# Kernel tuning notes

Measured on AMD Instinct MI355X. Metric: run time of the kernel, lower is better.

## Reference

```python
import jax, jax.numpy as jnp
import numpy as np

N_CLASSES = 18

def setup_inputs() -> dict:
    key = jax.random.key(0)
    k1, k2 = jax.random.split(key)
    B = 2_000_000
    output = jax.random.normal(k1, (B, N_CLASSES), dtype=jnp.float32)
    labels_soft = jax.random.uniform(k2, (B, N_CLASSES), dtype=jnp.float32)
    return {"output": output, "labels_soft": labels_soft}

def reference(output, labels_soft):
    # Original: sum over classes of mean_b( CE(output, cls) * labels_soft[:, cls] )
    # = mean over batch of sum_c( -log_softmax(output)[b, c] * labels_soft[b, c] )
    logp = jax.nn.log_softmax(output, axis=-1)          # [B, C]
    per_row = -jnp.sum(logp * labels_soft, axis=-1)     # [B]
    return jnp.mean(per_row)
```

## Files before the change

kernel.cpp:

```cpp
#include <hip/hip_runtime.h>

#define NCLS 18
#define RPC 128
#define CHF (RPC * NCLS)
#define CHF4 (CHF / 4)
#define WPB 4
#define GRID_A 1024

__global__ __launch_bounds__(256) void ce_soft_kernel(
    const float4* __restrict__ X4,
    const float4* __restrict__ L4,
    float* __restrict__ partials,
    int B)
{
    __shared__ float s[WPB][CHF];

    const int t    = threadIdx.x;
    const int lane = t & 63;
    const int wid  = t >> 6;
    const int gw   = blockIdx.x * WPB + wid;
    const int nw   = gridDim.x * WPB;
    const int nChunks = B / RPC;

    float acc = 0.0f;

    for (int ch = gw; ch < nChunks; ch += nw) {
        const size_t g4 = (size_t)ch * CHF4;
        float4 v[9];

        #pragma unroll
        for (int j = 0; j < 9; ++j) v[j] = X4[g4 + (size_t)(j * 64 + lane)];
        #pragma unroll
        for (int j = 0; j < 9; ++j) *(float4*)&s[wid][(j * 64 + lane) * 4] = v[j];
        __builtin_amdgcn_wave_barrier();

        float x0[NCLS], x1[NCLS];
        {
            const float2* r0 = (const float2*)&s[wid][(2 * lane)     * NCLS];
            const float2* r1 = (const float2*)&s[wid][(2 * lane + 1) * NCLS];
            #pragma unroll
            for (int j = 0; j < 9; ++j) {
                float2 a = r0[j]; x0[2*j] = a.x; x0[2*j+1] = a.y;
                float2 b = r1[j]; x1[2*j] = b.x; x1[2*j+1] = b.y;
            }
        }
        __builtin_amdgcn_wave_barrier();

        #pragma unroll
        for (int j = 0; j < 9; ++j) v[j] = L4[g4 + (size_t)(j * 64 + lane)];
        #pragma unroll
        for (int j = 0; j < 9; ++j) *(float4*)&s[wid][(j * 64 + lane) * 4] = v[j];

        float se0 = 0.0f, se1 = 0.0f;
        #pragma unroll
        for (int c = 0; c < NCLS; ++c) { se0 += __expf(x0[c]); se1 += __expf(x1[c]); }

        __builtin_amdgcn_wave_barrier();

        float dot0 = 0.0f, sl0 = 0.0f, dot1 = 0.0f, sl1 = 0.0f;
        {
            const float2* r0 = (const float2*)&s[wid][(2 * lane)     * NCLS];
            const float2* r1 = (const float2*)&s[wid][(2 * lane + 1) * NCLS];
            #pragma unroll
            for (int j = 0; j < 9; ++j) {
                float2 a = r0[j];
                dot0 = fmaf(a.x, x0[2*j], dot0); dot0 = fmaf(a.y, x0[2*j+1], dot0);
                sl0 += a.x + a.y;
                float2 b = r1[j];
                dot1 = fmaf(b.x, x1[2*j], dot1); dot1 = fmaf(b.y, x1[2*j+1], dot1);
                sl1 += b.x + b.y;
            }
        }
        acc += fmaf(sl0, __logf(se0), -dot0) + fmaf(sl1, __logf(se1), -dot1);
        __builtin_amdgcn_wave_barrier();
    }

    const float2* X2 = (const float2*)X4;
    const float2* L2 = (const float2*)L4;
    for (int row = nChunks * RPC + gw * 64 + lane; row < B; row += nw * 64) {
        float x[NCLS], l[NCLS];
        #pragma unroll
        for (int j = 0; j < 9; ++j) { float2 a = X2[(size_t)row * 9 + j]; x[2*j] = a.x; x[2*j+1] = a.y; }
        #pragma unroll
        for (int j = 0; j < 9; ++j) { float2 b = L2[(size_t)row * 9 + j]; l[2*j] = b.x; l[2*j+1] = b.y; }
        float se = 0.0f, dot = 0.0f, sl = 0.0f;
        #pragma unroll
        for (int c = 0; c < NCLS; ++c) { se += __expf(x[c]); dot = fmaf(l[c], x[c], dot); sl += l[c]; }
        acc += fmaf(sl, __logf(se), -dot);
    }

    #pragma unroll
    for (int off = 32; off > 0; off >>= 1) acc += __shfl_down(acc, off, 64);

    __shared__ float wsum[WPB];
    if (lane == 0) wsum[wid] = acc;
    __syncthreads();
    if (t == 0) partials[blockIdx.x] = wsum[0] + wsum[1] + wsum[2] + wsum[3];
}

__global__ __launch_bounds__(256) void ce_reduce_kernel(
    const float* __restrict__ partials, float* __restrict__ out, int n, float invB)
{
    float acc = 0.0f;
    for (int i = threadIdx.x; i < n; i += 256) acc += partials[i];

    #pragma unroll
    for (int off = 32; off > 0; off >>= 1) acc += __shfl_down(acc, off, 64);

    __shared__ float wave_sums[4];
    const int lane = threadIdx.x & 63;
    const int wid  = threadIdx.x >> 6;
    if (lane == 0) wave_sums[wid] = acc;
    __syncthreads();
    if (threadIdx.x == 0)
        out[0] = (wave_sums[0] + wave_sums[1] + wave_sums[2] + wave_sums[3]) * invB;
}

extern "C" void kernel_launch(void* const* d_in, const int* in_sizes, int n_in,
                              void* d_out, int out_size, void* d_ws, size_t ws_size,
                              hipStream_t stream) {
    const float4* X4 = (const float4*)d_in[0];
    const float4* L4 = (const float4*)d_in[1];
    float* partials = (float*)d_ws;
    float* result = (float*)d_out;

    int B = in_sizes[0] / NCLS;

    ce_soft_kernel<<<GRID_A, 256, 0, stream>>>(X4, L4, partials, B);
    ce_reduce_kernel<<<1, 256, 0, stream>>>(partials, result, GRID_A, 1.0f / (float)B);
}
```

Baseline: 294.1 us.

## Split loss into flat dot-product stream and per-row label-sum times logsumexp

Decomposes the soft cross-entropy into a global dot(logits, labels) computed by a flat coalesced float4 streaming kernel, plus a per-row kernel that only computes sum(labels)*log(sum(exp(logits))). The intent is to shorten the per-row dependency chain and lower register pressure, and to make the dot product a simple bandwidth-friendly stream. In exchange both inputs are read from memory twice. The final result now subtracts one large global sum from another, which increases cancellation error.

```diff
diff --git a/kernel.cpp b/kernel.cpp
--- a/kernel.cpp
+++ b/kernel.cpp
@@ -5,12 +5,49 @@
 #define CHF (RPC * NCLS)
 #define CHF4 (CHF / 4)
 #define WPB 4
-#define GRID_A 1024
+#define GRID_R 1024
+#define GRID_P 2048
 
-__global__ __launch_bounds__(256) void ce_soft_kernel(
+__global__ __launch_bounds__(256) void ce_dot_stream(
     const float4* __restrict__ X4,
     const float4* __restrict__ L4,
-    float* __restrict__ partials,
+    float* __restrict__ pdot,
+    int n4)
+{
+    const int tid = blockIdx.x * 256 + threadIdx.x;
+    const int stride = gridDim.x * 256;
+
+    float a0 = 0.0f, a1 = 0.0f;
+    int i = tid;
+    for (; i + stride < n4; i += 2 * stride) {
+        float4 x0 = X4[i],          l0 = L4[i];
+        float4 x1 = X4[i + stride], l1 = L4[i + stride];
+        a0 = fmaf(x0.x, l0.x, a0); a0 = fmaf(x0.y, l0.y, a0);
+        a0 = fmaf(x0.z, l0.z, a0); a0 = fmaf(x0.w, l0.w, a0);
+        a1 = fmaf(x1.x, l1.x, a1); a1 = fmaf(x1.y, l1.y, a1);
+        a1 = fmaf(x1.z, l1.z, a1); a1 = fmaf(x1.w, l1.w, a1);
+    }
+    for (; i < n4; i += stride) {
+        float4 x = X4[i], l = L4[i];
+        a0 = fmaf(x.x, l.x, a0); a0 = fmaf(x.y, l.y, a0);
+        a0 = fmaf(x.z, l.z, a0); a0 = fmaf(x.w, l.w, a0);
+    }
+    float acc = a0 + a1;
+
+    #pragma unroll
+    for (int off = 32; off > 0; off >>= 1) acc += __shfl_down(acc, off, 64);
+
+    __shared__ float wsum[4];
+    const int lane = threadIdx.x & 63, wid = threadIdx.x >> 6;
+    if (lane == 0) wsum[wid] = acc;
+    __syncthreads();
+    if (threadIdx.x == 0) pdot[blockIdx.x] = wsum[0] + wsum[1] + wsum[2] + wsum[3];
+}
+
+__global__ __launch_bounds__(256) void ce_sllse(
+    const float4* __restrict__ X4,
+    const float4* __restrict__ L4,
+    float* __restrict__ psl,
     int B)
 {
     __shared__ float s[WPB][CHF];
@@ -34,14 +71,14 @@
         for (int j = 0; j < 9; ++j) *(float4*)&s[wid][(j * 64 + lane) * 4] = v[j];
         __builtin_amdgcn_wave_barrier();
 
-        float x0[NCLS], x1[NCLS];
+        float se0 = 0.0f, se1 = 0.0f;
         {
             const float2* r0 = (const float2*)&s[wid][(2 * lane)     * NCLS];
             const float2* r1 = (const float2*)&s[wid][(2 * lane + 1) * NCLS];
             #pragma unroll
             for (int j = 0; j < 9; ++j) {
-                float2 a = r0[j]; x0[2*j] = a.x; x0[2*j+1] = a.y;
-                float2 b = r1[j]; x1[2*j] = b.x; x1[2*j+1] = b.y;
+                float2 a = r0[j]; se0 += __expf(a.x) + __expf(a.y);
+                float2 b = r1[j]; se1 += __expf(b.x) + __expf(b.y);
             }
         }
         __builtin_amdgcn_wave_barrier();
@@ -51,42 +88,35 @@
         #pragma unroll
         for (int j = 0; j < 9; ++j) *(float4*)&s[wid][(j * 64 + lane) * 4] = v[j];
 
-        float se0 = 0.0f, se1 = 0.0f;
-        #pragma unroll
-        for (int c = 0; c < NCLS; ++c) { se0 += __expf(x0[c]); se1 += __expf(x1[c]); }
+        float lg0 = __logf(se0), lg1 = __logf(se1);
 
         __builtin_amdgcn_wave_barrier();
 
-        float dot0 = 0.0f, sl0 = 0.0f, dot1 = 0.0f, sl1 = 0.0f;
+        float sl0 = 0.0f, sl1 = 0.0f;
         {
             const float2* r0 = (const float2*)&s[wid][(2 * lane)     * NCLS];
             const float2* r1 = (const float2*)&s[wid][(2 * lane + 1) * NCLS];
             #pragma unroll
             for (int j = 0; j < 9; ++j) {
-                float2 a = r0[j];
-                dot0 = fmaf(a.x, x0[2*j], dot0); dot0 = fmaf(a.y, x0[2*j+1], dot0);
-                sl0 += a.x + a.y;
-                float2 b = r1[j];
-                dot1 = fmaf(b.x, x1[2*j], dot1); dot1 = fmaf(b.y, x1[2*j+1], dot1);
-                sl1 += b.x + b.y;
+                float2 a = r0[j]; sl0 += a.x + a.y;
+                float2 b = r1[j]; sl1 += b.x + b.y;
             }
         }
-        acc += fmaf(sl0, __logf(se0), -dot0) + fmaf(sl1, __logf(se1), -dot1);
+        acc = fmaf(sl0, lg0, acc);
+        acc = fmaf(sl1, lg1, acc);
         __builtin_amdgcn_wave_barrier();
     }
 
     const float2* X2 = (const float2*)X4;
     const float2* L2 = (const float2*)L4;
     for (int row = nChunks * RPC + gw * 64 + lane; row < B; row += nw * 64) {
-        float x[NCLS], l[NCLS];
+        float se = 0.0f, sl = 0.0f;
         #pragma unroll
-        for (int j = 0; j < 9; ++j) { float2 a = X2[(size_t)row * 9 + j]; x[2*j] = a.x; x[2*j+1] = a.y; }
-        #pragma unroll
-        for (int j = 0; j < 9; ++j) { float2 b = L2[(size_t)row * 9 + j]; l[2*j] = b.x; l[2*j+1] = b.y; }
-        float se = 0.0f, dot = 0.0f, sl = 0.0f;
-        #pragma unroll
-        for (int c = 0; c < NCLS; ++c) { se += __expf(x[c]); dot = fmaf(l[c], x[c], dot); sl += l[c]; }
-        acc += fmaf(sl, __logf(se), -dot);
+        for (int j = 0; j < 9; ++j) {
+            float2 a = X2[(size_t)row * 9 + j]; se += __expf(a.x) + __expf(a.y);
+            float2 b = L2[(size_t)row * 9 + j]; sl += b.x + b.y;
+        }
+        acc = fmaf(sl, __logf(se), acc);
     }
 
     #pragma unroll
@@ -95,25 +125,27 @@
     __shared__ float wsum[WPB];
     if (lane == 0) wsum[wid] = acc;
     __syncthreads();
-    if (t == 0) partials[blockIdx.x] = wsum[0] + wsum[1] + wsum[2] + wsum[3];
+    if (t == 0) psl[blockIdx.x] = wsum[0] + wsum[1] + wsum[2] + wsum[3];
 }
 
-__global__ __launch_bounds__(256) void ce_reduce_kernel(
-    const float* __restrict__ partials, float* __restrict__ out, int n, float invB)
+__global__ __launch_bounds__(256) void ce_final(
+    const float* __restrict__ pdot, int ndot,
+    const float* __restrict__ psl, int nsl,
+    float* __restrict__ out, float invB)
 {
     float acc = 0.0f;
-    for (int i = threadIdx.x; i < n; i += 256) acc += partials[i];
+    for (int i = threadIdx.x; i < nsl; i += 256) acc += psl[i];
+    for (int i = threadIdx.x; i < ndot; i += 256) acc -= pdot[i];
 
     #pragma unroll
     for (int off = 32; off > 0; off >>= 1) acc += __shfl_down(acc, off, 64);
 
-    __shared__ float wave_sums[4];
-    const int lane = threadIdx.x & 63;
-    const int wid  = threadIdx.x >> 6;
-    if (lane == 0) wave_sums[wid] = acc;
+    __shared__ float wsum[4];
+    const int lane = threadIdx.x & 63, wid = threadIdx.x >> 6;
+    if (lane == 0) wsum[wid] = acc;
     __syncthreads();
     if (threadIdx.x == 0)
-        out[0] = (wave_sums[0] + wave_sums[1] + wave_sums[2] + wave_sums[3]) * invB;
+        out[0] = (wsum[0] + wsum[1] + wsum[2] + wsum[3]) * invB;
 }
 
 extern "C" void kernel_launch(void* const* d_in, const int* in_sizes, int n_in,
@@ -121,11 +153,14 @@
                               hipStream_t stream) {
     const float4* X4 = (const float4*)d_in[0];
     const float4* L4 = (const float4*)d_in[1];
-    float* partials = (float*)d_ws;
+    float* pdot = (float*)d_ws;
+    float* psl  = (float*)d_ws + GRID_P;
     float* result = (float*)d_out;
 
-    int B = in_sizes[0] / NCLS;
+    int B  = in_sizes[0] / NCLS;
+    int n4 = in_sizes[0] / 4;
 
-    ce_soft_kernel<<<GRID_A, 256, 0, stream>>>(X4, L4, partials, B);
-    ce_reduce_kernel<<<1, 256, 0, stream>>>(partials, result, GRID_A, 1.0f / (float)B);
+    ce_dot_stream<<<GRID_P, 256, 0, stream>>>(X4, L4, pdot, n4);
+    ce_sllse<<<GRID_R, 256, 0, stream>>>(X4, L4, psl, B);
+    ce_final<<<1, 256, 0, stream>>>(pdot, GRID_P, psl, GRID_R, result, 1.0f / (float)B);
 }
```

Measured after the change: 335.3 us. 14.0% more time.
